# Kernel tuning notes

Hardware: AMD Instinct MI355X
Metric: run time of the kernel (lower is better)

The kernel has to match this reference:

```python
import jax, jax.numpy as jnp
import numpy as np

B, L, D = 64, 512, 768

def setup_inputs() -> dict:
    key = jax.random.key(0)
    k1, k2, k3, k4 = jax.random.split(key, 4)
    hidden_states = jax.random.normal(k1, (B, L, D), dtype=jnp.float32)
    # nn.Linear(hidden_size, hidden_size): weight [D, D], bias [D]
    W = jax.random.normal(k2, (D, D), dtype=jnp.float32) * (1.0 / np.sqrt(D))
    b = jax.random.normal(k3, (D,), dtype=jnp.float32) * 0.02
    # context_vector: [D, 1]
    context_vector = jax.random.normal(k4, (D, 1), dtype=jnp.float32)
    return {"hidden_states": hidden_states, "W": W, "b": b, "context_vector": context_vector}

def reference(hidden_states, W, b, context_vector):
    # tanh(dense(h)): [B, L, D]; torch Linear uses x @ W.T + b
    proj = jnp.tanh(jnp.einsum('bld,ed->ble', hidden_states, W) + b)
    # scores: [B, L]
    scores = jnp.einsum('bld,d->bl', proj, context_vector[:, 0])
    # softmax over sequence dim (dim=1)
    attention_weights = jax.nn.softmax(scores, axis=1)
    # weighted sum over sequence: [B, D]
    weighted_output = jnp.einsum('bld,bl->bd', hidden_states, attention_weights)
    return (weighted_output, attention_weights)
```

## Files before the change

### kernel.cpp

```cpp
#include <hip/hip_runtime.h>
#include <hip/hip_bf16.h>


using half8 = __attribute__((ext_vector_type(8))) _Float16;
using f32x4 = __attribute__((ext_vector_type(4))) float;

#define AS1 __attribute__((address_space(1)))
#define AS3 __attribute__((address_space(3)))

__device__ __forceinline__ void gload_lds16(const void* g, void* l) {
  __builtin_amdgcn_global_load_lds((const AS1 void*)g, (AS3 void*)l, 16, 0, 0);
}

__device__ __forceinline__ unsigned short f2h(float x) {
  _Float16 h = (_Float16)x;
  return __builtin_bit_cast(unsigned short, h);
}

__device__ __forceinline__ float tanh_fast(float x) {
  return 1.0f - __fdividef(2.0f, 1.0f + __expf(2.0f * x));
}

__global__ void convert_w(const float4* __restrict__ W4, ushort4* __restrict__ Wt) {
  int i = blockIdx.x * 256 + threadIdx.x;
  float4 x = W4[i];
  ushort4 o;
  o.x = f2h(x.x); o.y = f2h(x.y); o.z = f2h(x.z); o.w = f2h(x.w);
  Wt[i] = o;
}

__global__ __launch_bounds__(256) void gemm_scores(
    const float* __restrict__ H, const ushort* __restrict__ Wt,
    const float* __restrict__ bias, const float* __restrict__ cvec,
    float* __restrict__ part) {
  __shared__ ushort ldsA[2][4096];
  __shared__ ushort ldsB[2][4096];
  __shared__ float scpart[2][128];

  const int tid = threadIdx.x;
  const int lane = tid & 63;
  const int wid = tid >> 6;
  const int wr = wid >> 1, wc = wid & 1;
  const int m = lane & 15, q = lane >> 4;

  const int bid = blockIdx.x;
  const int xcd = bid & 7;
  const int slot = bid >> 3;
  const int mtile = xcd * 32 + slot / 6;
  const int ntile = slot % 6;

  const char* const Bbase = (const char*)Wt + (size_t)(ntile * 128) * 1536;

  const int up = (tid & 7) ^ ((tid >> 3) & 7);
  const int lr_s = tid >> 3;
  const size_t src0 = (size_t)((up >> 2) * 64 + lr_s) * 1536 + (up & 3) * 16;
  const size_t src1 = (size_t)((up >> 2) * 64 + 32 + lr_s) * 1536 + (up & 3) * 16;
  const int wavebase = wid << 10;

  const int arow = tid >> 1, kh = tid & 1;
  const float4* const asrc =
      (const float4*)(H + (size_t)(mtile * 128 + arow) * 768) + kh * 4;
  const int a_lr = arow & 63, a_half = arow >> 6;
  const int wbyte0 = a_lr * 128 + (((a_half * 4 + kh * 2 + 0) ^ (a_lr & 7)) << 4);
  const int wbyte1 = a_lr * 128 + (((a_half * 4 + kh * 2 + 1) ^ (a_lr & 7)) << 4);

  f32x4 acc[4][4];
  #pragma unroll
  for (int i = 0; i < 4; ++i)
    #pragma unroll
    for (int j = 0; j < 4; ++j)
      acc[i][j] = (f32x4){0.f, 0.f, 0.f, 0.f};

  const int aslot = ((wr * 4 + q) ^ (m & 7)) * 16;
  const int bslot = ((wc * 4 + q) ^ (m & 7)) * 16;

  auto cvt8 = [](float4 u, float4 v) -> half8 {
    half8 r;
    r[0] = (_Float16)u.x; r[1] = (_Float16)u.y;
    r[2] = (_Float16)u.z; r[3] = (_Float16)u.w;
    r[4] = (_Float16)v.x; r[5] = (_Float16)v.y;
    r[6] = (_Float16)v.z; r[7] = (_Float16)v.w;
    return r;
  };

  float4 a_in[4];
  #pragma unroll
  for (int c = 0; c < 4; ++c) a_in[c] = asrc[c];
  gload_lds16(Bbase + src0, (char*)ldsB[0] + wavebase);
  gload_lds16(Bbase + src1, (char*)ldsB[0] + 4096 + wavebase);
  *(half8*)((char*)ldsA[0] + wbyte0) = cvt8(a_in[0], a_in[1]);
  *(half8*)((char*)ldsA[0] + wbyte1) = cvt8(a_in[2], a_in[3]);
  __syncthreads();

  #pragma unroll
  for (int t = 0; t < 24; ++t) {
    const int cur = t & 1, nxt = cur ^ 1;
    if (t < 23) {
      #pragma unroll
      for (int c = 0; c < 4; ++c) a_in[c] = asrc[(t + 1) * 8 + c];
      gload_lds16(Bbase + src0 + (t + 1) * 64, (char*)ldsB[nxt] + wavebase);
      gload_lds16(Bbase + src1 + (t + 1) * 64, (char*)ldsB[nxt] + 4096 + wavebase);
    }
    {
      const char* Ab = (const char*)ldsA[cur];
      const char* Bb = (const char*)ldsB[cur];
      half8 areg[4], breg[4];
      #pragma unroll
      for (int mi = 0; mi < 4; ++mi)
        areg[mi] = *(const half8*)(Ab + (mi * 16 + m) * 128 + aslot);
      #pragma unroll
      for (int ni = 0; ni < 4; ++ni)
        breg[ni] = *(const half8*)(Bb + (ni * 16 + m) * 128 + bslot);
      #pragma unroll
      for (int mi = 0; mi < 4; ++mi)
        #pragma unroll
        for (int ni = 0; ni < 4; ++ni)
          acc[mi][ni] = __builtin_amdgcn_mfma_f32_16x16x32_f16(
              areg[mi], breg[ni], acc[mi][ni], 0, 0, 0);
    }
    if (t < 23) {
      *(half8*)((char*)ldsA[nxt] + wbyte0) = cvt8(a_in[0], a_in[1]);
      *(half8*)((char*)ldsA[nxt] + wbyte1) = cvt8(a_in[2], a_in[3]);
    }
    __syncthreads();
  }

  float bb[4], cc[4];
  #pragma unroll
  for (int ni = 0; ni < 4; ++ni) {
    int e = ntile * 128 + wc * 64 + ni * 16 + m;
    bb[ni] = bias[e];
    cc[ni] = cvec[e];
  }
  #pragma unroll
  for (int mi = 0; mi < 4; ++mi) {
    #pragma unroll
    for (int j = 0; j < 4; ++j) {
      float s = 0.f;
      #pragma unroll
      for (int ni = 0; ni < 4; ++ni)
        s += tanh_fast(acc[mi][ni][j] + bb[ni]) * cc[ni];
      s += __shfl_xor(s, 1);
      s += __shfl_xor(s, 2);
      s += __shfl_xor(s, 4);
      s += __shfl_xor(s, 8);
      if (m == 0) scpart[wc][wr * 64 + mi * 16 + q * 4 + j] = s;
    }
  }
  __syncthreads();
  if (tid < 128)
    part[ntile * 32768 + mtile * 128 + tid] = scpart[0][tid] + scpart[1][tid];
}

__global__ void wsum_fused(const float* __restrict__ H, const float* __restrict__ prt,
                           float* __restrict__ out) {
  int b = blockIdx.x, dc = blockIdx.y;
  int t = threadIdx.x;
  __shared__ float w[512];
  __shared__ float redm[2], reds[2];

  float s[4];
  #pragma unroll
  for (int i = 0; i < 4; ++i) {
    int r = b * 512 + t + i * 128;
    s[i] = prt[r] + prt[32768 + r] + prt[2 * 32768 + r] +
           prt[3 * 32768 + r] + prt[4 * 32768 + r] + prt[5 * 32768 + r];
  }
  float mx = fmaxf(fmaxf(s[0], s[1]), fmaxf(s[2], s[3]));
  #pragma unroll
  for (int o = 32; o >= 1; o >>= 1) mx = fmaxf(mx, __shfl_xor(mx, o));
  if ((t & 63) == 0) redm[t >> 6] = mx;
  __syncthreads();
  mx = fmaxf(redm[0], redm[1]);

  float e[4], sm = 0.f;
  #pragma unroll
  for (int i = 0; i < 4; ++i) { e[i] = __expf(s[i] - mx); sm += e[i]; }
  #pragma unroll
  for (int o = 32; o >= 1; o >>= 1) sm += __shfl_xor(sm, o);
  if ((t & 63) == 0) reds[t >> 6] = sm;
  __syncthreads();
  float inv = 1.0f / (reds[0] + reds[1]);
  #pragma unroll
  for (int i = 0; i < 4; ++i) w[t + i * 128] = e[i] * inv;
  __syncthreads();

  int d0 = dc * 256 + t * 2;
  const float2* hp = (const float2*)(H + (size_t)b * 512 * 768 + d0);
  float a0 = 0.f, a1 = 0.f;
  #pragma unroll 8
  for (int l = 0; l < 512; ++l) {
    float2 u = hp[(size_t)l * 384];
    float wl = w[l];
    a0 += wl * u.x;
    a1 += wl * u.y;
  }
  out[b * 768 + d0] = a0;
  out[b * 768 + d0 + 1] = a1;

  if (dc == 0) {
    #pragma unroll
    for (int i = 0; i < 4; ++i)
      out[49152 + b * 512 + t + i * 128] = w[t + i * 128];
  }
}

extern "C" void kernel_launch(void* const* d_in, const int* in_sizes, int n_in,
                              void* d_out, int out_size, void* d_ws, size_t ws_size,
                              hipStream_t stream) {
  const float* H    = (const float*)d_in[0];
  const float* W    = (const float*)d_in[1];
  const float* bias = (const float*)d_in[2];
  const float* cvec = (const float*)d_in[3];
  float* out = (float*)d_out;

  char* ws = (char*)d_ws;
  ushort* Wt = (ushort*)(ws + 0);
  float*  prt = (float*)(ws + 1179648);

  hipLaunchKernelGGL(convert_w, dim3(576), dim3(256), 0, stream,
                     (const float4*)W, (ushort4*)Wt);
  hipLaunchKernelGGL(gemm_scores, dim3(1536), dim3(256), 0, stream,
                     H, Wt, bias, cvec, prt);
  hipLaunchKernelGGL(wsum_fused, dim3(64, 3), dim3(128), 0, stream,
                     H, prt, out);
}
```

Baseline: 114.9 us.

## Stage fp32 activations directly into LDS via async global-to-LDS loads

The A operand (hidden states) is now copied as raw fp32 into LDS with global_load_lds DMA instead of being loaded into registers, converted to fp16 and written by threads. The fp32-to-fp16 conversion moves to the LDS read side right before the MFMAs, and MFMA issue is wrapped in s_setprio. This frees VGPRs and removes the register round trip on the load path. In exchange the A tile in LDS doubles in size and each wave does twice the LDS reads plus conversion per k-step.

```diff
diff --git a/kernel.cpp b/kernel.cpp
--- a/kernel.cpp
+++ b/kernel.cpp
@@ -33,7 +33,7 @@
     const float* __restrict__ H, const ushort* __restrict__ Wt,
     const float* __restrict__ bias, const float* __restrict__ cvec,
     float* __restrict__ part) {
-  __shared__ ushort ldsA[2][4096];
+  __shared__ float  ldsA[2][4096];
   __shared__ ushort ldsB[2][4096];
   __shared__ float scpart[2][128];
 
@@ -49,20 +49,17 @@
   const int mtile = xcd * 32 + slot / 6;
   const int ntile = slot % 6;
 
+  const char* const Abase = (const char*)(H + (size_t)(mtile * 128) * 768);
   const char* const Bbase = (const char*)Wt + (size_t)(ntile * 128) * 1536;
 
-  const int up = (tid & 7) ^ ((tid >> 3) & 7);
-  const int lr_s = tid >> 3;
-  const size_t src0 = (size_t)((up >> 2) * 64 + lr_s) * 1536 + (up & 3) * 16;
-  const size_t src1 = (size_t)((up >> 2) * 64 + 32 + lr_s) * 1536 + (up & 3) * 16;
+  const int tr3 = tid >> 3;
+  const int au = (tid & 7) ^ (tr3 & 7);
+  const size_t asrc0 = (size_t)tr3 * 3072 + au * 16;
+
+  const int up = (tid & 7) ^ (tr3 & 7);
+  const size_t bsrc0 = (size_t)((up >> 2) * 64 + tr3) * 1536 + (up & 3) * 16;
+  const size_t bsrc1 = (size_t)((up >> 2) * 64 + 32 + tr3) * 1536 + (up & 3) * 16;
   const int wavebase = wid << 10;
-
-  const int arow = tid >> 1, kh = tid & 1;
-  const float4* const asrc =
-      (const float4*)(H + (size_t)(mtile * 128 + arow) * 768) + kh * 4;
-  const int a_lr = arow & 63, a_half = arow >> 6;
-  const int wbyte0 = a_lr * 128 + (((a_half * 4 + kh * 2 + 0) ^ (a_lr & 7)) << 4);
-  const int wbyte1 = a_lr * 128 + (((a_half * 4 + kh * 2 + 1) ^ (a_lr & 7)) << 4);
 
   f32x4 acc[4][4];
   #pragma unroll
@@ -71,57 +68,53 @@
     for (int j = 0; j < 4; ++j)
       acc[i][j] = (f32x4){0.f, 0.f, 0.f, 0.f};
 
-  const int aslot = ((wr * 4 + q) ^ (m & 7)) * 16;
+  auto stage = [&](int kt, int s) {
+    #pragma unroll
+    for (int c = 0; c < 4; ++c)
+      gload_lds16(Abase + asrc0 + (size_t)c * 98304 + kt * 128,
+                  (char*)ldsA[s] + c * 4096 + wavebase);
+    gload_lds16(Bbase + bsrc0 + kt * 64, (char*)ldsB[s] + wavebase);
+    gload_lds16(Bbase + bsrc1 + kt * 64, (char*)ldsB[s] + 4096 + wavebase);
+  };
+
+  const int aoff0 = ((2 * q) ^ (m & 7)) * 16;
   const int bslot = ((wc * 4 + q) ^ (m & 7)) * 16;
 
-  auto cvt8 = [](float4 u, float4 v) -> half8 {
-    half8 r;
-    r[0] = (_Float16)u.x; r[1] = (_Float16)u.y;
-    r[2] = (_Float16)u.z; r[3] = (_Float16)u.w;
-    r[4] = (_Float16)v.x; r[5] = (_Float16)v.y;
-    r[6] = (_Float16)v.z; r[7] = (_Float16)v.w;
-    return r;
-  };
-
-  float4 a_in[4];
-  #pragma unroll
-  for (int c = 0; c < 4; ++c) a_in[c] = asrc[c];
-  gload_lds16(Bbase + src0, (char*)ldsB[0] + wavebase);
-  gload_lds16(Bbase + src1, (char*)ldsB[0] + 4096 + wavebase);
-  *(half8*)((char*)ldsA[0] + wbyte0) = cvt8(a_in[0], a_in[1]);
-  *(half8*)((char*)ldsA[0] + wbyte1) = cvt8(a_in[2], a_in[3]);
-  __syncthreads();
-
-  #pragma unroll
-  for (int t = 0; t < 24; ++t) {
-    const int cur = t & 1, nxt = cur ^ 1;
-    if (t < 23) {
-      #pragma unroll
-      for (int c = 0; c < 4; ++c) a_in[c] = asrc[(t + 1) * 8 + c];
-      gload_lds16(Bbase + src0 + (t + 1) * 64, (char*)ldsB[nxt] + wavebase);
-      gload_lds16(Bbase + src1 + (t + 1) * 64, (char*)ldsB[nxt] + 4096 + wavebase);
+  auto compute = [&](int s) {
+    const char* Ab = (const char*)ldsA[s];
+    const char* Bb = (const char*)ldsB[s];
+    half8 areg[4], breg[4];
+    #pragma unroll
+    for (int mi = 0; mi < 4; ++mi) {
+      int rowb = (wr * 64 + mi * 16 + m) * 128;
+      f32x4 lo = *(const f32x4*)(Ab + rowb + aoff0);
+      f32x4 hi = *(const f32x4*)(Ab + rowb + (aoff0 ^ 16));
+      half8 r;
+      r[0] = (_Float16)lo[0]; r[1] = (_Float16)lo[1];
+      r[2] = (_Float16)lo[2]; r[3] = (_Float16)lo[3];
+      r[4] = (_Float16)hi[0]; r[5] = (_Float16)hi[1];
+      r[6] = (_Float16)hi[2]; r[7] = (_Float16)hi[3];
+      areg[mi] = r;
     }
-    {
-      const char* Ab = (const char*)ldsA[cur];
-      const char* Bb = (const char*)ldsB[cur];
-      half8 areg[4], breg[4];
-      #pragma unroll
-      for (int mi = 0; mi < 4; ++mi)
-        areg[mi] = *(const half8*)(Ab + (mi * 16 + m) * 128 + aslot);
+    #pragma unroll
+    for (int ni = 0; ni < 4; ++ni)
+      breg[ni] = *(const half8*)(Bb + (ni * 16 + m) * 128 + bslot);
+    __builtin_amdgcn_s_setprio(1);
+    #pragma unroll
+    for (int mi = 0; mi < 4; ++mi)
       #pragma unroll
       for (int ni = 0; ni < 4; ++ni)
-        breg[ni] = *(const half8*)(Bb + (ni * 16 + m) * 128 + bslot);
-      #pragma unroll
-      for (int mi = 0; mi < 4; ++mi)
-        #pragma unroll
-        for (int ni = 0; ni < 4; ++ni)
-          acc[mi][ni] = __builtin_amdgcn_mfma_f32_16x16x32_f16(
-              areg[mi], breg[ni], acc[mi][ni], 0, 0, 0);
-    }
-    if (t < 23) {
-      *(half8*)((char*)ldsA[nxt] + wbyte0) = cvt8(a_in[0], a_in[1]);
-      *(half8*)((char*)ldsA[nxt] + wbyte1) = cvt8(a_in[2], a_in[3]);
-    }
+        acc[mi][ni] = __builtin_amdgcn_mfma_f32_16x16x32_f16(
+            areg[mi], breg[ni], acc[mi][ni], 0, 0, 0);
+    __builtin_amdgcn_s_setprio(0);
+  };
+
+  stage(0, 0);
+  __syncthreads();
+  #pragma unroll
+  for (int t = 0; t < 24; ++t) {
+    if (t < 23) stage(t + 1, (t + 1) & 1);
+    compute(t & 1);
     __syncthreads();
   }
 
```

Measured after the change: 105.4 us, median of 2. 1.09x faster.
